# Kernel tuning notes

Measured on AMD Instinct MI355X. Metric: run time of the kernel, lower is better.

The kernel has to match this reference:

```python
import jax, jax.numpy as jnp
import numpy as np

S, B, D, H = 512, 256, 256, 256  # seq, batch, input_dim, hidden_dim
E = D + H                        # attention embed dim


def setup_inputs() -> dict:
    key = jax.random.key(0)
    ks = jax.random.split(key, 9)
    w = lambda k, shape: (jax.random.normal(k, shape, jnp.float32) * 0.02)
    return {
        "inputs": jax.random.normal(ks[0], (S, B, D), jnp.float32),
        "Wq": w(ks[1], (E, E)),
        "Wk": w(ks[2], (E, E)),
        "Wv": w(ks[3], (E, E)),
        "Wf": w(ks[4], (H, E)), "bf": jnp.zeros((H,), jnp.float32),
        "Wi": w(ks[5], (H, E)), "bi": jnp.zeros((H,), jnp.float32),
        "Wg": w(ks[6], (H, E)), "bg": jnp.zeros((H,), jnp.float32),
        "Wo": w(ks[7], (H, E)), "bo": jnp.zeros((H,), jnp.float32),
    }


def reference(inputs, Wq, Wk, Wv, Wf, bf, Wi, bi, Wg, bg, Wo, bo):
    seq, batch, d_in = inputs.shape
    h_dim = Wf.shape[0]
    scale = 1.0 / np.sqrt(d_in + h_dim)

    def step(carry, x):
        hx, cx = carry
        comb = jnp.concatenate([x, hx], axis=1)            # (B, E)
        q = comb @ Wq.T
        k = comb @ Wk.T
        v = comb @ Wv.T
        # NOTE: attention is over the batch dimension, as in the source.
        scores = jax.nn.softmax((q @ k.T) * scale, axis=-1)  # (B, B)
        attn = scores @ v                                    # (B, E)
        f = jax.nn.sigmoid(attn @ Wf.T + bf)
        i = jax.nn.sigmoid(attn @ Wi.T + bi)
        g = jnp.tanh(attn @ Wg.T + bg)
        o = jax.nn.sigmoid(attn @ Wo.T + bo)
        cx_new = f * cx + i * g
        hx_new = o * jnp.tanh(cx_new)
        return (hx_new, cx_new), hx_new

    init = (jnp.zeros((batch, h_dim), inputs.dtype),
            jnp.zeros((batch, h_dim), inputs.dtype))
    (hx, cx), stacked = jax.lax.scan(step, init, inputs)
    return stacked, (hx, cx)
```

## Files before the change

### kernel.cpp

```cpp
#include <hip/hip_runtime.h>
#include <hip/hip_bf16.h>


typedef __hip_bfloat16 bf16;
typedef __attribute__((ext_vector_type(8))) short bf16x8;
typedef __attribute__((ext_vector_type(4))) float f32x4;
typedef unsigned long long u64;

#define SEQ 512
#define BB  256
#define DD  256
#define HH  256
#define EE  512
#define QK_SCALE 0.04419417382415922f

#define WS_COMB0  0
#define WS_COMB1  262144
#define WS_COMBT0 524288
#define WS_COMBT1 786432
#define WS_CX     1048576
#define WS_MT     1310720
#define WS_UF     1835008
#define WS_UI     2097152
#define WS_UG     2359296
#define WS_UO     2621440
#define WS_END    2883584

__device__ __forceinline__ float sigm(float x) { return 1.0f / (1.0f + __expf(-x)); }

__device__ __forceinline__ unsigned short f2bf_s(float f) {
  bf16 h = __float2bfloat16(f);
  return *reinterpret_cast<unsigned short*>(&h);
}
__device__ __forceinline__ u64 pack4(float a, float b, float c, float d) {
  union { unsigned short s[4]; u64 u; } x;
  x.s[0] = f2bf_s(a); x.s[1] = f2bf_s(b); x.s[2] = f2bf_s(c); x.s[3] = f2bf_s(d);
  return x.u;
}

__global__ void __launch_bounds__(256) qlstm_init_kernel(
    const float* __restrict__ x,
    const float* __restrict__ Wq, const float* __restrict__ Wk, const float* __restrict__ Wv,
    const float* __restrict__ Wf, const float* __restrict__ Wi,
    const float* __restrict__ Wg, const float* __restrict__ Wo,
    char* __restrict__ wsb)
{
  const int gid = blockIdx.x * blockDim.x + threadIdx.x;
  bf16* comb0  = (bf16*)(wsb + WS_COMB0);
  bf16* combT0 = (bf16*)(wsb + WS_COMBT0);
  float* cx    = (float*)(wsb + WS_CX);
  bf16* mt     = (bf16*)(wsb + WS_MT);

  if (gid < 65536) {
    const int i = gid >> 8, e = gid & 255;
    const bf16 xv = __float2bfloat16(x[i * DD + e]);
    comb0[i * EE + e] = xv;
    comb0[i * EE + 256 + e] = __float2bfloat16(0.0f);
    combT0[e * BB + i] = xv;
    combT0[(256 + e) * BB + i] = __float2bfloat16(0.0f);
  } else {
    cx[gid - 65536] = 0.0f;
  }

  #pragma unroll 1
  for (int kk = 0; kk < 2; ++kk) {
    const int o = gid + kk * 131072;
    const int n = o >> 9, e = o & 511;
    float acc = 0.0f;
    #pragma unroll 4
    for (int j = 0; j < 512; ++j) acc = __builtin_fmaf(Wq[j * 512 + e], Wk[j * 512 + n], acc);
    mt[o] = __float2bfloat16(acc);
  }
  const float* srcs[4] = { Wf, Wi, Wg, Wo };
  const int offs[4] = { WS_UF, WS_UI, WS_UG, WS_UO };
  #pragma unroll 1
  for (int a = 0; a < 4; ++a) {
    bf16* U = (bf16*)(wsb + offs[a]);
    const float* W = srcs[a];
    const int h = gid >> 9, e = gid & 511;
    float acc = 0.0f;
    #pragma unroll 4
    for (int ep = 0; ep < 512; ++ep) acc = __builtin_fmaf(W[h * 512 + ep], Wv[ep * 512 + e], acc);
    U[gid] = __float2bfloat16(acc);
  }
}

__global__ void __launch_bounds__(1024) qlstm_step_kernel(
    const float* __restrict__ x,
    const float* __restrict__ bfv, const float* __restrict__ biv,
    const float* __restrict__ bgv, const float* __restrict__ bov,
    float* __restrict__ out, char* __restrict__ wsb, int t)
{
  const int par = t & 1;
  const bf16* comb   = (const bf16*)(wsb + (par ? WS_COMB1 : WS_COMB0));
  const bf16* combT  = (const bf16*)(wsb + (par ? WS_COMBT1 : WS_COMBT0));
  bf16* combN  = (bf16*)(wsb + (par ? WS_COMB0 : WS_COMB1));
  bf16* combTN = (bf16*)(wsb + (par ? WS_COMBT0 : WS_COMBT1));
  float* cx_ws = (float*)(wsb + WS_CX);
  const bf16* mt   = (const bf16*)(wsb + WS_MT);
  const bf16* uf_b = (const bf16*)(wsb + WS_UF);
  const bf16* ui_b = (const bf16*)(wsb + WS_UI);
  const bf16* ug_b = (const bf16*)(wsb + WS_UG);
  const bf16* uo_b = (const bf16*)(wsb + WS_UO);

  const int wg   = blockIdx.x;
  const int s    = wg >> 2;
  const int q4   = wg & 3;
  const int r0   = s * 16;
  const int tid  = threadIdx.x;
  const int wid  = tid >> 6;
  const int lane = tid & 63;
  const int l16  = lane & 15;
  const int kq   = lane >> 4;

  __shared__ unsigned short c_lds[16 * 520];
  __shared__ unsigned short z_lds[16 * 520];
  __shared__ unsigned short a_lds[16 * 520];
  __shared__ float          s_lds[16 * 256];
  __shared__ unsigned short p_lds[16 * 264];
  __shared__ float          g_lds[16 * 256];
  __shared__ unsigned short ht_lds[64 * 18];

  {
    const int row = tid >> 6, c8 = (tid & 63) * 8;
    *(bf16x8*)(&c_lds[row * 520 + c8]) =
        *(const bf16x8*)(comb + (size_t)(r0 + row) * EE + c8);
  }
  __syncthreads();

  #pragma unroll
  for (int h2 = 0; h2 < 2; ++h2) {
    const int n0 = (wid * 2 + h2) * 16;
    const bf16* arow = mt + (size_t)(n0 + l16) * EE;
    const unsigned short* brow = &c_lds[l16 * 520];
    f32x4 acc = {0.f, 0.f, 0.f, 0.f};
    #pragma unroll
    for (int half = 0; half < 2; ++half) {
      bf16x8 mfr[8];
      #pragma unroll
      for (int u = 0; u < 8; ++u)
        mfr[u] = *(const bf16x8*)(arow + (half * 8 + u) * 32 + kq * 8);
      #pragma unroll
      for (int u = 0; u < 8; ++u) {
        bf16x8 bf8 = *(const bf16x8*)(brow + (half * 8 + u) * 32 + kq * 8);
        acc = __builtin_amdgcn_mfma_f32_16x16x32_bf16(mfr[u], bf8, acc, 0, 0, 0);
      }
    }
    *(u64*)(&z_lds[l16 * 520 + n0 + kq * 4]) = pack4(acc[0], acc[1], acc[2], acc[3]);
  }
  __syncthreads();
  {
    const int j0 = wid * 16;
    const unsigned short* arow = &z_lds[l16 * 520];
    const bf16* brow = comb + (size_t)(j0 + l16) * EE;
    f32x4 acc = {0.f, 0.f, 0.f, 0.f};
    #pragma unroll
    for (int half = 0; half < 2; ++half) {
      bf16x8 cfr[8];
      #pragma unroll
      for (int u = 0; u < 8; ++u)
        cfr[u] = *(const bf16x8*)(brow + (half * 8 + u) * 32 + kq * 8);
      #pragma unroll
      for (int u = 0; u < 8; ++u) {
        bf16x8 af = *(const bf16x8*)(arow + (half * 8 + u) * 32 + kq * 8);
        acc = __builtin_amdgcn_mfma_f32_16x16x32_bf16(af, cfr[u], acc, 0, 0, 0);
      }
    }
    #pragma unroll
    for (int r = 0; r < 4; ++r)
      s_lds[(kq * 4 + r) * 256 + j0 + l16] = acc[r];
  }
  __syncthreads();
  {
    const int i = wid;
    const float4 v = *(const float4*)(&s_lds[i * 256 + lane * 4]);
    float m = fmaxf(fmaxf(v.x, v.y), fmaxf(v.z, v.w));
    #pragma unroll
    for (int off = 32; off > 0; off >>= 1) m = fmaxf(m, __shfl_xor(m, off));
    float e0 = __expf((v.x - m) * QK_SCALE);
    float e1 = __expf((v.y - m) * QK_SCALE);
    float e2 = __expf((v.z - m) * QK_SCALE);
    float e3 = __expf((v.w - m) * QK_SCALE);
    float sum = e0 + e1 + e2 + e3;
    #pragma unroll
    for (int off = 32; off > 0; off >>= 1) sum += __shfl_xor(sum, off);
    const float rinv = 1.0f / sum;
    unsigned short* pp = &p_lds[i * 264 + lane * 4];
    pp[0] = f2bf_s(e0 * rinv);
    pp[1] = f2bf_s(e1 * rinv);
    pp[2] = f2bf_s(e2 * rinv);
    pp[3] = f2bf_s(e3 * rinv);
  }
  __syncthreads();
  #pragma unroll
  for (int q8 = 0; q8 < 2; ++q8) {
    const int n0 = wid * 16 + q8 * 256;
    const bf16* arow = combT + (size_t)(n0 + l16) * BB;
    const unsigned short* brow = &p_lds[l16 * 264];
    f32x4 acc = {0.f, 0.f, 0.f, 0.f};
    bf16x8 tfr[8];
    #pragma unroll
    for (int u = 0; u < 8; ++u)
      tfr[u] = *(const bf16x8*)(arow + u * 32 + kq * 8);
    #pragma unroll
    for (int u = 0; u < 8; ++u) {
      bf16x8 bf8 = *(const bf16x8*)(brow + u * 32 + kq * 8);
      acc = __builtin_amdgcn_mfma_f32_16x16x32_bf16(tfr[u], bf8, acc, 0, 0, 0);
    }
    *(u64*)(&a_lds[l16 * 520 + n0 + kq * 4]) = pack4(acc[0], acc[1], acc[2], acc[3]);
  }
  __syncthreads();
  {
    const int g   = wid >> 2;
    const int hcb = wid & 3;
    const int h0  = q4 * 64 + hcb * 16;
    const bf16* U = (g == 0) ? uf_b : (g == 1) ? ui_b : (g == 2) ? ug_b : uo_b;
    const unsigned short* arow = &a_lds[l16 * 520];
    const bf16* brow = U + (size_t)(h0 + l16) * EE;
    f32x4 acc = {0.f, 0.f, 0.f, 0.f};
    #pragma unroll
    for (int half = 0; half < 2; ++half) {
      bf16x8 ufr[8];
      #pragma unroll
      for (int u = 0; u < 8; ++u)
        ufr[u] = *(const bf16x8*)(brow + (half * 8 + u) * 32 + kq * 8);
      #pragma unroll
      for (int u = 0; u < 8; ++u) {
        bf16x8 af = *(const bf16x8*)(arow + (half * 8 + u) * 32 + kq * 8);
        acc = __builtin_amdgcn_mfma_f32_16x16x32_bf16(af, ufr[u], acc, 0, 0, 0);
      }
    }
    #pragma unroll
    for (int r = 0; r < 4; ++r)
      g_lds[wid * 256 + (kq * 4 + r) * 16 + l16] = acc[r];
  }
  __syncthreads();
  {
    const int hcb2 = tid >> 8;
    const int idx  = tid & 255;
    const int i    = idx >> 4, c = idx & 15;
    const int colg = q4 * 64 + hcb2 * 16 + c;
    const float F = sigm(g_lds[(0 * 4 + hcb2) * 256 + idx] + bfv[colg]);
    const float I = sigm(g_lds[(1 * 4 + hcb2) * 256 + idx] + biv[colg]);
    const float G = tanhf(g_lds[(2 * 4 + hcb2) * 256 + idx] + bgv[colg]);
    const float O = sigm(g_lds[(3 * 4 + hcb2) * 256 + idx] + bov[colg]);
    float* cxp = cx_ws + (size_t)wg * 1024 + tid;
    const float c2 = F * (*cxp) + I * G;
    const float h  = O * tanhf(c2);
    *cxp = c2;
    out[(size_t)t * 65536 + (size_t)(r0 + i) * 256 + colg] = h;
    const bf16 hb = __float2bfloat16(h);
    if (t < SEQ - 1) {
      combN[(size_t)(r0 + i) * EE + 256 + colg] = hb;
      ht_lds[(hcb2 * 16 + c) * 18 + i] = *reinterpret_cast<const unsigned short*>(&hb);
    } else {
      out[(size_t)SEQ * 65536 + (size_t)(r0 + i) * 256 + colg] = h;
      out[(size_t)SEQ * 65536 + 65536 + (size_t)(r0 + i) * 256 + colg] = c2;
    }
  }
  __syncthreads();
  if (t < SEQ - 1) {
    if (tid < 128) {
      const int row64 = tid >> 1, half = tid & 1;
      const int e = 256 + q4 * 64 + row64;
      *(u64*)(combTN + (size_t)e * BB + r0 + half * 8) =
          *(const u64*)(&ht_lds[row64 * 18 + half * 8]);
      *(u64*)(combTN + (size_t)e * BB + r0 + half * 8 + 4) =
          *(const u64*)(&ht_lds[row64 * 18 + half * 8 + 4]);
    }
    if (q4 == 0) {
      unsigned short* xT = c_lds;
      {
        const int i2 = tid >> 6, e4 = (tid & 63) * 4;
        const float4 xf = *(const float4*)(x + ((size_t)(t + 1) * BB + r0 + i2) * DD + e4);
        const u64 p = pack4(xf.x, xf.y, xf.z, xf.w);
        const unsigned short* ps = (const unsigned short*)&p;
        xT[(e4 + 0) * 18 + i2] = ps[0];
        xT[(e4 + 1) * 18 + i2] = ps[1];
        xT[(e4 + 2) * 18 + i2] = ps[2];
        xT[(e4 + 3) * 18 + i2] = ps[3];
        *(u64*)(combN + (size_t)(r0 + i2) * EE + e4) = p;
      }
      __syncthreads();
      if (tid < 512) {
        const int row = tid >> 1, half = tid & 1;
        *(u64*)(combTN + (size_t)row * BB + r0 + half * 8) =
            *(const u64*)(&xT[row * 18 + half * 8]);
        *(u64*)(combTN + (size_t)row * BB + r0 + half * 8 + 4) =
            *(const u64*)(&xT[row * 18 + half * 8 + 4]);
      }
    }
  }
}

extern "C" void kernel_launch(void* const* d_in, const int* in_sizes, int n_in,
                              void* d_out, int out_size, void* d_ws, size_t ws_size,
                              hipStream_t stream) {
  const float* x   = (const float*)d_in[0];
  const float* Wq  = (const float*)d_in[1];
  const float* Wk  = (const float*)d_in[2];
  const float* Wv  = (const float*)d_in[3];
  const float* Wf  = (const float*)d_in[4];
  const float* bfv = (const float*)d_in[5];
  const float* Wi  = (const float*)d_in[6];
  const float* biv = (const float*)d_in[7];
  const float* Wgg = (const float*)d_in[8];
  const float* bgv = (const float*)d_in[9];
  const float* Wo  = (const float*)d_in[10];
  const float* bov = (const float*)d_in[11];
  float* out = (float*)d_out;
  char* wsb = (char*)d_ws;

  hipLaunchKernelGGL(qlstm_init_kernel, dim3(512), dim3(256), 0, stream,
                     x, Wq, Wk, Wv, Wf, Wi, Wgg, Wo, wsb);

  for (int t = 0; t < SEQ; ++t) {
    hipLaunchKernelGGL(qlstm_step_kernel, dim3(64), dim3(1024), 0, stream,
                       x, bfv, biv, bgv, bov, out, wsb, t);
  }
}
```

Before: 20.86 ms.

## Run eight timesteps per launch with a software grid barrier between steps

Each step-kernel launch now loops over eight timesteps. Between steps it synchronises the 64 workgroups with a flag-based global barrier, which cuts the number of launches from 512 to 64. Cross-workgroup state (comb and combT) is written with agent-scope atomic stores and read with cache-bypassing loads so other workgroups see fresh values. The risks are spin-wait cost, a deadlock if all 64 workgroups are not co-resident, and the cost of the coherent loads.

```diff
diff --git a/kernel.cpp b/kernel.cpp
--- a/kernel.cpp
+++ b/kernel.cpp
@@ -8,10 +8,12 @@
 typedef unsigned long long u64;
 
 #define SEQ 512
+#define NSTEP 8
 #define BB  256
 #define DD  256
 #define HH  256
 #define EE  512
+#define NWG 64
 #define QK_SCALE 0.04419417382415922f
 
 #define WS_COMB0  0
@@ -24,7 +26,9 @@
 #define WS_UI     2097152
 #define WS_UG     2359296
 #define WS_UO     2621440
-#define WS_END    2883584
+#define WS_FLAGS  2883584
+#define WS_REL    2887680
+#define WS_END    2888192
 
 __device__ __forceinline__ float sigm(float x) { return 1.0f / (1.0f + __expf(-x)); }
 
@@ -36,6 +40,40 @@
   union { unsigned short s[4]; u64 u; } x;
   x.s[0] = f2bf_s(a); x.s[1] = f2bf_s(b); x.s[2] = f2bf_s(c); x.s[3] = f2bf_s(d);
   return x.u;
+}
+__device__ __forceinline__ void sta8(void* p, u64 v) {
+  __hip_atomic_store((u64*)p, v, __ATOMIC_RELAXED, __HIP_MEMORY_SCOPE_AGENT);
+}
+__device__ __forceinline__ unsigned lda4(const unsigned* p) {
+  return __hip_atomic_load(p, __ATOMIC_RELAXED, __HIP_MEMORY_SCOPE_AGENT);
+}
+__device__ __forceinline__ void sta4(unsigned* p, unsigned v) {
+  __hip_atomic_store(p, v, __ATOMIC_RELAXED, __HIP_MEMORY_SCOPE_AGENT);
+}
+#define LOAD16_COH(dst, addr) \
+  asm volatile("global_load_dwordx4 %0, %1, off sc0 sc1" : "=v"(dst) : "v"(addr))
+
+__device__ __forceinline__ void gbar64(unsigned* flags, unsigned* rel,
+                                       int wg, unsigned val) {
+  asm volatile("s_waitcnt vmcnt(0)" ::: "memory");
+  __syncthreads();
+  const int tid = threadIdx.x;
+  if (wg == NWG - 1) {
+    if (tid < 64) {
+      if (tid == 0) sta4(&flags[(NWG - 1) * 16], val);
+      if (tid < NWG) {
+        while (lda4(&flags[tid * 16]) < val) __builtin_amdgcn_s_sleep(1);
+      }
+    }
+    __syncthreads();
+    if (tid < 8) sta4(&rel[tid * 16], val);
+  } else {
+    if (tid == 0) {
+      sta4(&flags[wg * 16], val);
+      while (lda4(&rel[(wg & 7) * 16]) < val) __builtin_amdgcn_s_sleep(1);
+    }
+  }
+  __syncthreads();
 }
 
 __global__ void __launch_bounds__(256) qlstm_init_kernel(
@@ -61,6 +99,7 @@
   } else {
     cx[gid - 65536] = 0.0f;
   }
+  if (gid < (WS_END - WS_FLAGS) / 4) ((unsigned*)(wsb + WS_FLAGS))[gid] = 0u;
 
   #pragma unroll 1
   for (int kk = 0; kk < 2; ++kk) {
@@ -89,19 +128,16 @@
     const float* __restrict__ x,
     const float* __restrict__ bfv, const float* __restrict__ biv,
     const float* __restrict__ bgv, const float* __restrict__ bov,
-    float* __restrict__ out, char* __restrict__ wsb, int t)
+    float* __restrict__ out, char* __restrict__ wsb, int t0, int bbase)
 {
-  const int par = t & 1;
-  const bf16* comb   = (const bf16*)(wsb + (par ? WS_COMB1 : WS_COMB0));
-  const bf16* combT  = (const bf16*)(wsb + (par ? WS_COMBT1 : WS_COMBT0));
-  bf16* combN  = (bf16*)(wsb + (par ? WS_COMB0 : WS_COMB1));
-  bf16* combTN = (bf16*)(wsb + (par ? WS_COMBT0 : WS_COMBT1));
   float* cx_ws = (float*)(wsb + WS_CX);
   const bf16* mt   = (const bf16*)(wsb + WS_MT);
   const bf16* uf_b = (const bf16*)(wsb + WS_UF);
   const bf16* ui_b = (const bf16*)(wsb + WS_UI);
   const bf16* ug_b = (const bf16*)(wsb + WS_UG);
   const bf16* uo_b = (const bf16*)(wsb + WS_UO);
+  unsigned* flags = (unsigned*)(wsb + WS_FLAGS);
+  unsigned* rel   = (unsigned*)(wsb + WS_REL);
 
   const int wg   = blockIdx.x;
   const int s    = wg >> 2;
@@ -121,175 +157,197 @@
   __shared__ float          g_lds[16 * 256];
   __shared__ unsigned short ht_lds[64 * 18];
 
-  {
-    const int row = tid >> 6, c8 = (tid & 63) * 8;
-    *(bf16x8*)(&c_lds[row * 520 + c8]) =
-        *(const bf16x8*)(comb + (size_t)(r0 + row) * EE + c8);
-  }
-  __syncthreads();
-
-  #pragma unroll
-  for (int h2 = 0; h2 < 2; ++h2) {
-    const int n0 = (wid * 2 + h2) * 16;
-    const bf16* arow = mt + (size_t)(n0 + l16) * EE;
-    const unsigned short* brow = &c_lds[l16 * 520];
-    f32x4 acc = {0.f, 0.f, 0.f, 0.f};
+  for (int k = 0; k < NSTEP; ++k) {
+    const int t = t0 + k;
+    const int par = t & 1;
+    const bf16* comb   = (const bf16*)(wsb + (par ? WS_COMB1 : WS_COMB0));
+    const bf16* combT  = (const bf16*)(wsb + (par ? WS_COMBT1 : WS_COMBT0));
+    bf16* combN  = (bf16*)(wsb + (par ? WS_COMB0 : WS_COMB1));
+    bf16* combTN = (bf16*)(wsb + (par ? WS_COMBT0 : WS_COMBT1));
+
+    {
+      const int row = tid >> 6, c8 = (tid & 63) * 8;
+      bf16x8 cv;
+      LOAD16_COH(cv, comb + (size_t)(r0 + row) * EE + c8);
+      asm volatile("s_waitcnt vmcnt(0)" ::: "memory");
+      *(bf16x8*)(&c_lds[row * 520 + c8]) = cv;
+    }
+    __syncthreads();
+
     #pragma unroll
-    for (int half = 0; half < 2; ++half) {
-      bf16x8 mfr[8];
+    for (int h2 = 0; h2 < 2; ++h2) {
+      const int n0 = (wid * 2 + h2) * 16;
+      const bf16* arow = mt + (size_t)(n0 + l16) * EE;
+      const unsigned short* brow = &c_lds[l16 * 520];
+      f32x4 acc = {0.f, 0.f, 0.f, 0.f};
+      #pragma unroll
+      for (int half = 0; half < 2; ++half) {
+        bf16x8 mfr[8];
+        #pragma unroll
+        for (int u = 0; u < 8; ++u)
+          mfr[u] = *(const bf16x8*)(arow + (half * 8 + u) * 32 + kq * 8);
+        #pragma unroll
+        for (int u = 0; u < 8; ++u) {
+          bf16x8 bf8 = *(const bf16x8*)(brow + (half * 8 + u) * 32 + kq * 8);
+          acc = __builtin_amdgcn_mfma_f32_16x16x32_bf16(mfr[u], bf8, acc, 0, 0, 0);
+        }
+      }
+      *(u64*)(&z_lds[l16 * 520 + n0 + kq * 4]) = pack4(acc[0], acc[1], acc[2], acc[3]);
+    }
+    __syncthreads();
+    {
+      const int j0 = wid * 16;
+      const unsigned short* arow = &z_lds[l16 * 520];
+      const bf16* brow = comb + (size_t)(j0 + l16) * EE;
+      f32x4 acc = {0.f, 0.f, 0.f, 0.f};
+      #pragma unroll
+      for (int half = 0; half < 2; ++half) {
+        bf16x8 cfr[8];
+        #pragma unroll
+        for (int u = 0; u < 8; ++u)
+          LOAD16_COH(cfr[u], brow + (half * 8 + u) * 32 + kq * 8);
+        asm volatile("s_waitcnt vmcnt(0)" ::: "memory");
+        __builtin_amdgcn_sched_barrier(0);
+        #pragma unroll
+        for (int u = 0; u < 8; ++u) {
+          bf16x8 af = *(const bf16x8*)(arow + (half * 8 + u) * 32 + kq * 8);
+          acc = __builtin_amdgcn_mfma_f32_16x16x32_bf16(af, cfr[u], acc, 0, 0, 0);
+        }
+      }
+      #pragma unroll
+      for (int r = 0; r < 4; ++r)
+        s_lds[(kq * 4 + r) * 256 + j0 + l16] = acc[r];
+    }
+    __syncthreads();
+    {
+      const int i = wid;
+      const float4 v = *(const float4*)(&s_lds[i * 256 + lane * 4]);
+      float m = fmaxf(fmaxf(v.x, v.y), fmaxf(v.z, v.w));
+      #pragma unroll
+      for (int off = 32; off > 0; off >>= 1) m = fmaxf(m, __shfl_xor(m, off));
+      float e0 = __expf((v.x - m) * QK_SCALE);
+      float e1 = __expf((v.y - m) * QK_SCALE);
+      float e2 = __expf((v.z - m) * QK_SCALE);
+      float e3 = __expf((v.w - m) * QK_SCALE);
+      float sum = e0 + e1 + e2 + e3;
+      #pragma unroll
+      for (int off = 32; off > 0; off >>= 1) sum += __shfl_xor(sum, off);
+      const float rinv = 1.0f / sum;
+      unsigned short* pp = &p_lds[i * 264 + lane * 4];
+      pp[0] = f2bf_s(e0 * rinv);
+      pp[1] = f2bf_s(e1 * rinv);
+      pp[2] = f2bf_s(e2 * rinv);
+      pp[3] = f2bf_s(e3 * rinv);
+    }
+    __syncthreads();
+    #pragma unroll
+    for (int q8 = 0; q8 < 2; ++q8) {
+      const int n0 = wid * 16 + q8 * 256;
+      const bf16* arow = combT + (size_t)(n0 + l16) * BB;
+      const unsigned short* brow = &p_lds[l16 * 264];
+      f32x4 acc = {0.f, 0.f, 0.f, 0.f};
+      bf16x8 tfr[8];
       #pragma unroll
       for (int u = 0; u < 8; ++u)
-        mfr[u] = *(const bf16x8*)(arow + (half * 8 + u) * 32 + kq * 8);
+        LOAD16_COH(tfr[u], arow + u * 32 + kq * 8);
+      asm volatile("s_waitcnt vmcnt(0)" ::: "memory");
+      __builtin_amdgcn_sched_barrier(0);
       #pragma unroll
       for (int u = 0; u < 8; ++u) {
-        bf16x8 bf8 = *(const bf16x8*)(brow + (half * 8 + u) * 32 + kq * 8);
-        acc = __builtin_amdgcn_mfma_f32_16x16x32_bf16(mfr[u], bf8, acc, 0, 0, 0);
-      }
-    }
-    *(u64*)(&z_lds[l16 * 520 + n0 + kq * 4]) = pack4(acc[0], acc[1], acc[2], acc[3]);
-  }
-  __syncthreads();
-  {
-    const int j0 = wid * 16;
-    const unsigned short* arow = &z_lds[l16 * 520];
-    const bf16* brow = comb + (size_t)(j0 + l16) * EE;
-    f32x4 acc = {0.f, 0.f, 0.f, 0.f};
-    #pragma unroll
-    for (int half = 0; half < 2; ++half) {
-      bf16x8 cfr[8];
-      #pragma unroll
-      for (int u = 0; u < 8; ++u)
-        cfr[u] = *(const bf16x8*)(brow + (half * 8 + u) * 32 + kq * 8);
-      #pragma unroll
-      for (int u = 0; u < 8; ++u) {
-        bf16x8 af = *(const bf16x8*)(arow + (half * 8 + u) * 32 + kq * 8);
-        acc = __builtin_amdgcn_mfma_f32_16x16x32_bf16(af, cfr[u], acc, 0, 0, 0);
-      }
-    }
-    #pragma unroll
-    for (int r = 0; r < 4; ++r)
-      s_lds[(kq * 4 + r) * 256 + j0 + l16] = acc[r];
-  }
-  __syncthreads();
-  {
-    const int i = wid;
-    const float4 v = *(const float4*)(&s_lds[i * 256 + lane * 4]);
-    float m = fmaxf(fmaxf(v.x, v.y), fmaxf(v.z, v.w));
-    #pragma unroll
-    for (int off = 32; off > 0; off >>= 1) m = fmaxf(m, __shfl_xor(m, off));
-    float e0 = __expf((v.x - m) * QK_SCALE);
-    float e1 = __expf((v.y - m) * QK_SCALE);
-    float e2 = __expf((v.z - m) * QK_SCALE);
-    float e3 = __expf((v.w - m) * QK_SCALE);
-    float sum = e0 + e1 + e2 + e3;
-    #pragma unroll
-    for (int off = 32; off > 0; off >>= 1) sum += __shfl_xor(sum, off);
-    const float rinv = 1.0f / sum;
-    unsigned short* pp = &p_lds[i * 264 + lane * 4];
-    pp[0] = f2bf_s(e0 * rinv);
-    pp[1] = f2bf_s(e1 * rinv);
-    pp[2] = f2bf_s(e2 * rinv);
-    pp[3] = f2bf_s(e3 * rinv);
-  }
-  __syncthreads();
-  #pragma unroll
-  for (int q8 = 0; q8 < 2; ++q8) {
-    const int n0 = wid * 16 + q8 * 256;
-    const bf16* arow = combT + (size_t)(n0 + l16) * BB;
-    const unsigned short* brow = &p_lds[l16 * 264];
-    f32x4 acc = {0.f, 0.f, 0.f, 0.f};
-    bf16x8 tfr[8];
-    #pragma unroll
-    for (int u = 0; u < 8; ++u)
-      tfr[u] = *(const bf16x8*)(arow + u * 32 + kq * 8);
-    #pragma unroll
-    for (int u = 0; u < 8; ++u) {
-      bf16x8 bf8 = *(const bf16x8*)(brow + u * 32 + kq * 8);
-      acc = __builtin_amdgcn_mfma_f32_16x16x32_bf16(tfr[u], bf8, acc, 0, 0, 0);
-    }
-    *(u64*)(&a_lds[l16 * 520 + n0 + kq * 4]) = pack4(acc[0], acc[1], acc[2], acc[3]);
-  }
-  __syncthreads();
-  {
-    const int g   = wid >> 2;
-    const int hcb = wid & 3;
-    const int h0  = q4 * 64 + hcb * 16;
-    const bf16* U = (g == 0) ? uf_b : (g == 1) ? ui_b : (g == 2) ? ug_b : uo_b;
-    const unsigned short* arow = &a_lds[l16 * 520];
-    const bf16* brow = U + (size_t)(h0 + l16) * EE;
-    f32x4 acc = {0.f, 0.f, 0.f, 0.f};
-    #pragma unroll
-    for (int half = 0; half < 2; ++half) {
-      bf16x8 ufr[8];
-      #pragma unroll
-      for (int u = 0; u < 8; ++u)
-        ufr[u] = *(const bf16x8*)(brow + (half * 8 + u) * 32 + kq * 8);
-      #pragma unroll
-      for (int u = 0; u < 8; ++u) {
-        bf16x8 af = *(const bf16x8*)(arow + (half * 8 + u) * 32 + kq * 8);
-        acc = __builtin_amdgcn_mfma_f32_16x16x32_bf16(af, ufr[u], acc, 0, 0, 0);
-      }
-    }
-    #pragma unroll
-    for (int r = 0; r < 4; ++r)
-      g_lds[wid * 256 + (kq * 4 + r) * 16 + l16] = acc[r];
-  }
-  __syncthreads();
-  {
-    const int hcb2 = tid >> 8;
-    const int idx  = tid & 255;
-    const int i    = idx >> 4, c = idx & 15;
-    const int colg = q4 * 64 + hcb2 * 16 + c;
-    const float F = sigm(g_lds[(0 * 4 + hcb2) * 256 + idx] + bfv[colg]);
-    const float I = sigm(g_lds[(1 * 4 + hcb2) * 256 + idx] + biv[colg]);
-    const float G = tanhf(g_lds[(2 * 4 + hcb2) * 256 + idx] + bgv[colg]);
-    const float O = sigm(g_lds[(3 * 4 + hcb2) * 256 + idx] + bov[colg]);
-    float* cxp = cx_ws + (size_t)wg * 1024 + tid;
-    const float c2 = F * (*cxp) + I * G;
-    const float h  = O * tanhf(c2);
-    *cxp = c2;
-    out[(size_t)t * 65536 + (size_t)(r0 + i) * 256 + colg] = h;
-    const bf16 hb = __float2bfloat16(h);
+        bf16x8 bf8 = *(const bf16x8*)(brow + u * 32 + kq * 8);
+        acc = __builtin_amdgcn_mfma_f32_16x16x32_bf16(tfr[u], bf8, acc, 0, 0, 0);
+      }
+      *(u64*)(&a_lds[l16 * 520 + n0 + kq * 4]) = pack4(acc[0], acc[1], acc[2], acc[3]);
+    }
+    __syncthreads();
+    {
+      const int g   = wid >> 2;
+      const int hcb = wid & 3;
+      const int h0  = q4 * 64 + hcb * 16;
+      const bf16* U = (g == 0) ? uf_b : (g == 1) ? ui_b : (g == 2) ? ug_b : uo_b;
+      const unsigned short* arow = &a_lds[l16 * 520];
+      const bf16* brow = U + (size_t)(h0 + l16) * EE;
+      f32x4 acc = {0.f, 0.f, 0.f, 0.f};
+      #pragma unroll
+      for (int half = 0; half < 2; ++half) {
+        bf16x8 ufr[8];
+        #pragma unroll
+        for (int u = 0; u < 8; ++u)
+          ufr[u] = *(const bf16x8*)(brow + (half * 8 + u) * 32 + kq * 8);
+        #pragma unroll
+        for (int u = 0; u < 8; ++u) {
+          bf16x8 af = *(const bf16x8*)(arow + (half * 8 + u) * 32 + kq * 8);
+          acc = __builtin_amdgcn_mfma_f32_16x16x32_bf16(af, ufr[u], acc, 0, 0, 0);
+        }
+      }
+      #pragma unroll
+      for (int r = 0; r < 4; ++r)
+        g_lds[wid * 256 + (kq * 4 + r) * 16 + l16] = acc[r];
+    }
+    __syncthreads();
+    {
+      const int hcb2 = tid >> 8;
+      const int idx  = tid & 255;
+      const int i    = idx >> 4, c = idx & 15;
+      const int colg = q4 * 64 + hcb2 * 16 + c;
+      const float F = sigm(g_lds[(0 * 4 + hcb2) * 256 + idx] + bfv[colg]);
+      const float I = sigm(g_lds[(1 * 4 + hcb2) * 256 + idx] + biv[colg]);
+      const float G = tanhf(g_lds[(2 * 4 + hcb2) * 256 + idx] + bgv[colg]);
+      const float O = sigm(g_lds[(3 * 4 + hcb2) * 256 + idx] + bov[colg]);
+      float* cxp = cx_ws + (size_t)wg * 1024 + tid;
+      const float c2 = F * (*cxp) + I * G;
+      const float h  = O * tanhf(c2);
+      *cxp = c2;
+      out[(size_t)t * 65536 + (size_t)(r0 + i) * 256 + colg] = h;
+      if (t < SEQ - 1) {
+        const bf16 hb = __float2bfloat16(h);
+        ht_lds[(hcb2 * 16 + c) * 18 + i] = *reinterpret_cast<const unsigned short*>(&hb);
+      } else {
+        out[(size_t)SEQ * 65536 + (size_t)(r0 + i) * 256 + colg] = h;
+        out[(size_t)SEQ * 65536 + 65536 + (size_t)(r0 + i) * 256 + colg] = c2;
+      }
+    }
+    __syncthreads();
     if (t < SEQ - 1) {
-      combN[(size_t)(r0 + i) * EE + 256 + colg] = hb;
-      ht_lds[(hcb2 * 16 + c) * 18 + i] = *reinterpret_cast<const unsigned short*>(&hb);
-    } else {
-      out[(size_t)SEQ * 65536 + (size_t)(r0 + i) * 256 + colg] = h;
-      out[(size_t)SEQ * 65536 + 65536 + (size_t)(r0 + i) * 256 + colg] = c2;
-    }
-  }
-  __syncthreads();
-  if (t < SEQ - 1) {
-    if (tid < 128) {
-      const int row64 = tid >> 1, half = tid & 1;
-      const int e = 256 + q4 * 64 + row64;
-      *(u64*)(combTN + (size_t)e * BB + r0 + half * 8) =
-          *(const u64*)(&ht_lds[row64 * 18 + half * 8]);
-      *(u64*)(combTN + (size_t)e * BB + r0 + half * 8 + 4) =
-          *(const u64*)(&ht_lds[row64 * 18 + half * 8 + 4]);
-    }
-    if (q4 == 0) {
-      unsigned short* xT = c_lds;
-      {
-        const int i2 = tid >> 6, e4 = (tid & 63) * 4;
-        const float4 xf = *(const float4*)(x + ((size_t)(t + 1) * BB + r0 + i2) * DD + e4);
-        const u64 p = pack4(xf.x, xf.y, xf.z, xf.w);
-        const unsigned short* ps = (const unsigned short*)&p;
-        xT[(e4 + 0) * 18 + i2] = ps[0];
-        xT[(e4 + 1) * 18 + i2] = ps[1];
-        xT[(e4 + 2) * 18 + i2] = ps[2];
-        xT[(e4 + 3) * 18 + i2] = ps[3];
-        *(u64*)(combN + (size_t)(r0 + i2) * EE + e4) = p;
-      }
-      __syncthreads();
-      if (tid < 512) {
-        const int row = tid >> 1, half = tid & 1;
-        *(u64*)(combTN + (size_t)row * BB + r0 + half * 8) =
-            *(const u64*)(&xT[row * 18 + half * 8]);
-        *(u64*)(combTN + (size_t)row * BB + r0 + half * 8 + 4) =
-            *(const u64*)(&xT[row * 18 + half * 8 + 4]);
-      }
-    }
+      if (tid < 256) {
+        const int i = tid >> 4, c4 = (tid & 15) * 4;
+        union { unsigned short sv[4]; u64 u; } pk;
+        #pragma unroll
+        for (int j = 0; j < 4; ++j) pk.sv[j] = ht_lds[(c4 + j) * 18 + i];
+        sta8(combN + (size_t)(r0 + i) * EE + 256 + q4 * 64 + c4, pk.u);
+      }
+      if (tid < 128) {
+        const int row64 = tid >> 1, half = tid & 1;
+        const int e = 256 + q4 * 64 + row64;
+        sta8(combTN + (size_t)e * BB + r0 + half * 8,
+             *(const u64*)(&ht_lds[row64 * 18 + half * 8]));
+        sta8(combTN + (size_t)e * BB + r0 + half * 8 + 4,
+             *(const u64*)(&ht_lds[row64 * 18 + half * 8 + 4]));
+      }
+      if (q4 == 0) {
+        unsigned short* xT = c_lds;
+        {
+          const int i2 = tid >> 6, e4 = (tid & 63) * 4;
+          const float4 xf = *(const float4*)(x + ((size_t)(t + 1) * BB + r0 + i2) * DD + e4);
+          const u64 p = pack4(xf.x, xf.y, xf.z, xf.w);
+          const unsigned short* ps = (const unsigned short*)&p;
+          xT[(e4 + 0) * 18 + i2] = ps[0];
+          xT[(e4 + 1) * 18 + i2] = ps[1];
+          xT[(e4 + 2) * 18 + i2] = ps[2];
+          xT[(e4 + 3) * 18 + i2] = ps[3];
+          sta8(combN + (size_t)(r0 + i2) * EE + e4, p);
+        }
+        __syncthreads();
+        if (tid < 512) {
+          const int row = tid >> 1, half = tid & 1;
+          sta8(combTN + (size_t)row * BB + r0 + half * 8,
+               *(const u64*)(&xT[row * 18 + half * 8]));
+          sta8(combTN + (size_t)row * BB + r0 + half * 8 + 4,
+               *(const u64*)(&xT[row * 18 + half * 8 + 4]));
+        }
+      }
+    }
+    if (k < NSTEP - 1) gbar64(flags, rel, wg, (unsigned)(bbase + k + 1));
   }
 }
 
@@ -314,8 +372,10 @@
   hipLaunchKernelGGL(qlstm_init_kernel, dim3(512), dim3(256), 0, stream,
                      x, Wq, Wk, Wv, Wf, Wi, Wgg, Wo, wsb);
 
-  for (int t = 0; t < SEQ; ++t) {
-    hipLaunchKernelGGL(qlstm_step_kernel, dim3(64), dim3(1024), 0, stream,
-                       x, bfv, biv, bgv, bov, out, wsb, t);
-  }
-}
+  for (int d = 0; d < SEQ / NSTEP; ++d) {
+    int t0 = d * NSTEP;
+    int bbase = d * (NSTEP - 1);
+    hipLaunchKernelGGL(qlstm_step_kernel, dim3(NWG), dim3(1024), 0, stream,
+                       x, bfv, biv, bgv, bov, out, wsb, t0, bbase);
+  }
+}
```

After: 21.14 ms. About the same (+1.3%).
